# Optimization experiments

Hardware: AMD Instinct MI355X
Metric: run time of the kernel (lower is better)

## Reference

```python
import jax, jax.numpy as jnp
import numpy as np

FEATURE_DIM = 256
NUM_HEADS = 4
HEAD_DIM = FEATURE_DIM // NUM_HEADS  # 64
B, N = 4, 2048


def _conv1x1(x, w, b):
    # x: [B, C_in, N], w: [C_out, C_in], b: [C_out] -> [B, C_out, N]
    return jnp.einsum('oc,bcn->bon', w, x) + b[None, :, None]


def setup_inputs() -> dict:
    key = jax.random.key(0)
    ks = jax.random.split(key, 11)
    std = 0.02
    d = {
        'query': jax.random.normal(ks[0], (B, FEATURE_DIM, N), jnp.float32),
        'key': jax.random.normal(ks[1], (B, FEATURE_DIM, N), jnp.float32),
        'value': jax.random.normal(ks[2], (B, FEATURE_DIM, N), jnp.float32),
        'wq': jax.random.normal(ks[3], (FEATURE_DIM, FEATURE_DIM), jnp.float32) * std,
        'bq': jnp.zeros((FEATURE_DIM,), jnp.float32),
        'wk': jax.random.normal(ks[4], (FEATURE_DIM, FEATURE_DIM), jnp.float32) * std,
        'bk': jnp.zeros((FEATURE_DIM,), jnp.float32),
        'wv': jax.random.normal(ks[5], (FEATURE_DIM, FEATURE_DIM), jnp.float32) * std,
        'bv': jnp.zeros((FEATURE_DIM,), jnp.float32),
        'wm': jax.random.normal(ks[6], (FEATURE_DIM, FEATURE_DIM), jnp.float32) * std,
        'bm': jnp.zeros((FEATURE_DIM,), jnp.float32),
    }
    return d


def reference(query, key, value, wq, bq, wk, bk, wv, bv, wm, bm):
    b = query.shape[0]
    # 1x1 conv projections, then split channels as (head_dim, num_heads) -- head_dim outer,
    # matching torch's .view(b, head_dim, num_heads, -1)
    q = _conv1x1(query, wq, bq).reshape(b, HEAD_DIM, NUM_HEADS, -1)
    k = _conv1x1(key, wk, bk).reshape(b, HEAD_DIM, NUM_HEADS, -1)
    v = _conv1x1(value, wv, bv).reshape(b, HEAD_DIM, NUM_HEADS, -1)
    scores = jnp.einsum('bdhn,bdhm->bhnm', q, k) / jnp.sqrt(jnp.asarray(HEAD_DIM, q.dtype))
    probs = jax.nn.softmax(scores, axis=-1)
    out = jnp.einsum('bhnm,bdhm->bdhn', probs, v)
    out = out.reshape(b, HEAD_DIM * NUM_HEADS, -1)
    return _conv1x1(out, wm, bm)
```

## Files before the change

### kernel.cpp

```cpp
#include <hip/hip_runtime.h>
#include <math.h>

#define B_ 4
#define C_ 256
#define N_ 2048
#define H_ 4
#define D_ 64

typedef __attribute__((ext_vector_type(8))) short bf16x8;
typedef __attribute__((ext_vector_type(4))) float f32x4;

#define QSCALE 0.18033688011112042f

__device__ __forceinline__ float fexp2(float x) {
#if __has_builtin(__builtin_amdgcn_exp2f)
    return __builtin_amdgcn_exp2f(x);
#else
    float r;
    asm("v_exp_f32 %0, %1\n\ts_nop 1" : "=v"(r) : "v"(x));
    return r;
#endif
}

__device__ __forceinline__ ushort f2bf(float x) {
    uint u = __float_as_uint(x);
    uint r = (u + 0x7fffu + ((u >> 16) & 1u)) >> 16;
    return (ushort)r;
}
__device__ __forceinline__ float bf2f(ushort u) {
    return __uint_as_float((uint)u << 16);
}
__device__ __forceinline__ uint4 pack8(const ushort* v) {
    uint4 r;
    r.x = (uint)v[0] | ((uint)v[1] << 16);
    r.y = (uint)v[2] | ((uint)v[3] << 16);
    r.z = (uint)v[4] | ((uint)v[5] << 16);
    r.w = (uint)v[6] | ((uint)v[7] << 16);
    return r;
}
__device__ __forceinline__ void glds16(const void* g, void* l) {
    __builtin_amdgcn_global_load_lds(
        (const __attribute__((address_space(1))) unsigned int*)g,
        (__attribute__((address_space(3))) unsigned int*)l, 16, 0, 0);
}

__global__ __launch_bounds__(256) void pack_w(const float* __restrict__ w0,
                                              const float* __restrict__ w1,
                                              const float* __restrict__ w2,
                                              const float* __restrict__ w3,
                                              ushort* __restrict__ Whimg,
                                              ushort* __restrict__ Wlimg) {
    const int ws = blockIdx.x;
    const int ks = blockIdx.y;
    const float* W = ws == 0 ? w0 : ws == 1 ? w1 : ws == 2 ? w2 : w3;
    ushort* Hh = Whimg + ws * 65536;
    ushort* Hl = Wlimg + ws * 65536;
    const int o  = threadIdx.x;
    const int of = o >> 4;
    const int li = o & 15;

    float v[32];
#pragma unroll
    for (int q = 0; q < 8; ++q)
        *(float4*)&v[q * 4] = *(const float4*)&W[o * 256 + ks * 32 + q * 4];

#pragma unroll
    for (int g = 0; g < 4; ++g) {
        ushort hi[8], lo[8];
#pragma unroll
        for (int e = 0; e < 8; ++e) {
            const float x = v[g * 8 + e];
            hi[e] = f2bf(x);
            lo[e] = f2bf(x - bf2f(hi[e]));
        }
        const size_t dst = ((size_t)(ks * 16 + of) * 64 + (g * 16 + li)) * 8;
        *(uint4*)(Hh + dst) = pack8(hi);
        if (ws == 3) *(uint4*)(Hl + dst) = pack8(lo);
    }
}

__global__ __launch_bounds__(256) void proj_fused(const float* __restrict__ Xq,
                                                  const float* __restrict__ Xk,
                                                  const float* __restrict__ Xv,
                                                  const ushort* __restrict__ Whimg,
                                                  const float* __restrict__ bq,
                                                  const float* __restrict__ bk,
                                                  const float* __restrict__ bv,
                                                  ushort* __restrict__ Qb,
                                                  ushort* __restrict__ Kimg,
                                                  ushort* __restrict__ Vimg) {
    __shared__ float  Xf[2][2048];
    __shared__ ushort Xb[2][2048];
    __shared__ ushort Ls[32][264];

    const int z   = blockIdx.z;
    const int sel = z >> 2, b = z & 3;
    const int nt  = blockIdx.x;
    const int n0  = nt * 32;
    const int tid  = threadIdx.x;
    const int wv   = tid >> 6;
    const int lane = tid & 63;
    const int li   = lane & 15;
    const int g    = lane >> 4;
    const int l7   = li & 7;

    const float* X = (sel == 0 ? Xq : sel == 1 ? Xk : Xv) + (size_t)b * C_ * N_;
    const ushort* Wh  = Whimg + sel * 65536;
    const float* bias = sel == 0 ? bq : sel == 1 ? bk : bv;

    const int st_row = wv * 16 + (lane >> 3);
    const int st_col = (lane & 7) * 4;

    const int cv_n  = tid & 31;
    const int cv_g  = tid >> 5;
    const int cv_c0 = cv_g * 8;
    const int cv_sl = (cv_g ^ (cv_n & 7)) * 8;

#define PSTAGE(buf, s_)                                                          \
    do {                                                                         \
        const float* p_ = X + (size_t)((s_) * 64 + st_row) * N_ + n0 + st_col;   \
        glds16(p_,          &Xf[buf][wv * 512]);                                 \
        glds16(p_ + 8 * N_, &Xf[buf][wv * 512 + 256]);                           \
    } while (0)

#define PCONV(dst, src)                                                          \
    do {                                                                         \
        ushort t_[8];                                                            \
        _Pragma("unroll")                                                        \
        for (int e = 0; e < 8; ++e)                                              \
            t_[e] = f2bf(Xf[src][(cv_c0 + e) * 32 + cv_n]);                      \
        *(uint4*)&Xb[dst][cv_n * 64 + cv_sl] = pack8(t_);                        \
    } while (0)

    PSTAGE(0, 0);
    __syncthreads();
    PSTAGE(1, 1);
    PCONV(0, 0);
    __syncthreads();

    const f32x4 zv = {0.f, 0.f, 0.f, 0.f};
    f32x4 acc[4][2] = {{zv, zv}, {zv, zv}, {zv, zv}, {zv, zv}};

    for (int st = 0; st < 4; ++st) {
        if (st + 2 < 4) PSTAGE(st & 1, st + 2);
        if (st + 1 < 4) PCONV((st + 1) & 1, (st + 1) & 1);

        bf16x8 xb[2][2];
#pragma unroll
        for (int nf = 0; nf < 2; ++nf)
#pragma unroll
            for (int ksub = 0; ksub < 2; ++ksub)
                xb[nf][ksub] = *(const bf16x8*)
                    &Xb[st & 1][(16 * nf + li) * 64 + 8 * (((ksub << 2) + g) ^ l7)];

        __builtin_amdgcn_s_setprio(1);
#pragma unroll
        for (int ksub = 0; ksub < 2; ++ksub) {
            const size_t ab = ((size_t)((2 * st + ksub) * 16 + wv * 4) * 64 + lane) * 8;
#pragma unroll
            for (int ot = 0; ot < 4; ++ot) {
                const bf16x8 ah = *(const bf16x8*)(Wh + ab + (size_t)ot * 512);
#pragma unroll
                for (int nf = 0; nf < 2; ++nf)
                    acc[ot][nf] = __builtin_amdgcn_mfma_f32_16x16x32_bf16(
                        ah, xb[nf][ksub], acc[ot][nf], 0, 0, 0);
            }
        }
        __builtin_amdgcn_s_setprio(0);
        __syncthreads();
    }

    const float scale = (sel == 0) ? QSCALE : 1.0f;
#pragma unroll
    for (int ot = 0; ot < 4; ++ot)
#pragma unroll
        for (int nf = 0; nf < 2; ++nf)
#pragma unroll
            for (int r = 0; r < 4; ++r) {
                const int o = wv * 64 + ot * 16 + g * 4 + r;
                Ls[nf * 16 + li][o] = f2bf((acc[ot][nf][r] + bias[o]) * scale);
            }
    __syncthreads();

    const int h  = tid >> 6;
    const int bh = b * 4 + h;
    if (sel == 0) {
#pragma unroll
        for (int r_ = 0; r_ < 4; ++r_) {
            const int gi = (tid & 63) + 64 * r_;
            const int n_l = gi >> 3, dr = gi & 7;
            ushort u[8];
#pragma unroll
            for (int e = 0; e < 8; ++e) u[e] = Ls[n_l][(dr * 8 + e) * 4 + h];
            *(uint4*)(Qb + (((size_t)bh * N_) + n0 + n_l) * 64 + dr * 8) = pack8(u);
        }
    } else if (sel == 1) {
#pragma unroll
        for (int r_ = 0; r_ < 4; ++r_) {
            const int gi = (tid & 63) + 64 * r_;
            const int n_l = gi >> 3, dr = gi & 7;
            ushort u[8];
#pragma unroll
            for (int e = 0; e < 8; ++e) u[e] = Ls[n_l][(dr * 8 + e) * 4 + h];
            const int jg    = n0 + n_l;
            const int j     = jg & 63;
            const int ktile = jg >> 6;
            *(uint4*)(Kimg + (((size_t)bh * 32 + ktile) << 12) + j * 64 +
                      ((dr * 8) ^ ((j & 7) << 3))) = pack8(u);
        }
    } else {
#pragma unroll
        for (int r_ = 0; r_ < 4; ++r_) {
            const int gi = (tid & 63) + 64 * r_;
            const int d = gi >> 2, jr = gi & 3;
            ushort u[8];
#pragma unroll
            for (int e = 0; e < 8; ++e) u[e] = Ls[jr * 8 + e][d * 4 + h];
            const int jbase = (nt & 1) * 32 + jr * 8;
            const int ktile = nt >> 1;
            *(uint4*)(Vimg + (((size_t)bh * 32 + ktile) << 12) + d * 64 +
                      (jbase ^ ((d & 7) << 3))) = pack8(u);
        }
    }
#undef PSTAGE
#undef PCONV
}

__global__ __launch_bounds__(256) void attn_v8(const ushort* __restrict__ Qb,
                                               const ushort* __restrict__ Kimg,
                                               const ushort* __restrict__ Vimg,
                                               float* __restrict__ Opart,
                                               float* __restrict__ lpart) {
    __shared__ ushort SMEM[24576];

    const int bid = blockIdx.x;
    const int L   = (bid & 7) * 64 + (bid >> 3);
    const int qt  = L & 15;
    const int ps  = L >> 4;
    const int bh  = ps >> 1;
    const int s   = ps & 1;

    const int tid  = threadIdx.x;
    const int wv   = tid >> 6;
    const int lane = tid & 63;
    const int li   = lane & 15;
    const int g    = lane >> 4;
    const int l7   = li & 7;
    const int i0w  = qt * 128 + wv * 32;

    bf16x8 qf[2][2];
#pragma unroll
    for (int qg = 0; qg < 2; ++qg)
#pragma unroll
        for (int ks = 0; ks < 2; ++ks)
            qf[qg][ks] = *(const bf16x8*)(Qb + ((size_t)bh * N_ + i0w + qg * 16 + li) * 64 +
                                          ks * 32 + g * 8);

    const ushort* Kg = Kimg + ((size_t)bh << 17);
    const ushort* Vg = Vimg + ((size_t)bh << 17);
    ushort* Pw = SMEM + 16384 + wv * 2048;

    const f32x4 z = {0.f, 0.f, 0.f, 0.f};
    f32x4 accO[4][2] = {{z, z}, {z, z}, {z, z}, {z, z}};
    f32x4 accL[2] = {z, z};
    const bf16x8 ones = {16256, 16256, 16256, 16256, 16256, 16256, 16256, 16256};

    const int kt0 = s * 16, kt1 = kt0 + 16;

#define STAGE(buf, kt_)                                                          \
    do {                                                                         \
        const ushort* ksrc = Kg + ((size_t)(kt_) << 12) + wv * 1024 + lane * 8;  \
        const ushort* vsrc = Vg + ((size_t)(kt_) << 12) + wv * 1024 + lane * 8;  \
        glds16(ksrc,       SMEM + (buf) * 4096 + wv * 1024);                     \
        glds16(ksrc + 512, SMEM + (buf) * 4096 + wv * 1024 + 512);               \
        glds16(vsrc,       SMEM + 8192 + (buf) * 4096 + wv * 1024);              \
        glds16(vsrc + 512, SMEM + 8192 + (buf) * 4096 + wv * 1024 + 512);        \
    } while (0)

    STAGE(0, kt0);

    int cur = 0;
    for (int kt = kt0; kt < kt1; ++kt) {
        if (kt + 1 < kt1) {
            STAGE(cur ^ 1, kt + 1);
            asm volatile("s_waitcnt vmcnt(4)" ::: "memory");
        } else {
            asm volatile("s_waitcnt vmcnt(0)" ::: "memory");
        }
        __builtin_amdgcn_s_barrier();

        const ushort* Kc = SMEM + cur * 4096;
        const ushort* Vc = SMEM + 8192 + cur * 4096;

        f32x4 sc[4][2];
        __builtin_amdgcn_s_setprio(1);
#pragma unroll
        for (int jt = 0; jt < 4; ++jt) {
            const ushort* row = Kc + (16 * jt + li) * 64;
            const bf16x8 kf0 = *(const bf16x8*)(row + 8 * (g ^ l7));
            const bf16x8 kf1 = *(const bf16x8*)(row + 8 * ((4 + g) ^ l7));
#pragma unroll
            for (int qg = 0; qg < 2; ++qg) {
                f32x4 a = z;
                a = __builtin_amdgcn_mfma_f32_16x16x32_bf16(kf0, qf[qg][0], a, 0, 0, 0);
                a = __builtin_amdgcn_mfma_f32_16x16x32_bf16(kf1, qf[qg][1], a, 0, 0, 0);
                sc[jt][qg] = a;
            }
        }
        __builtin_amdgcn_s_setprio(0);

#pragma unroll
        for (int qg = 0; qg < 2; ++qg) {
            const uint rowb = (uint)((qg * 16 + li) * 128);
#pragma unroll
            for (int jt = 0; jt < 4; ++jt) {
                const float p0 = fexp2(sc[jt][qg][0]);
                const float p1 = fexp2(sc[jt][qg][1]);
                const float p2 = fexp2(sc[jt][qg][2]);
                const float p3 = fexp2(sc[jt][qg][3]);
                const uint a01 = (__float_as_uint(p1) & 0xffff0000u) | (__float_as_uint(p0) >> 16);
                const uint a23 = (__float_as_uint(p3) & 0xffff0000u) | (__float_as_uint(p2) >> 16);
                const uint byteoff = rowb + (((uint)(jt * 32 + g * 8)) ^ ((uint)l7 << 4));
                *(uint2*)((char*)Pw + byteoff) = make_uint2(a01, a23);
            }
        }

        bf16x8 pf[2][2];
#pragma unroll
        for (int qg = 0; qg < 2; ++qg)
#pragma unroll
            for (int ks = 0; ks < 2; ++ks)
                pf[qg][ks] = *(const bf16x8*)((char*)Pw + (qg * 16 + li) * 128 +
                                              16 * ((4 * ks + g) ^ l7));

        __builtin_amdgcn_s_setprio(1);
#pragma unroll
        for (int qg = 0; qg < 2; ++qg) {
            accL[qg] = __builtin_amdgcn_mfma_f32_16x16x32_bf16(ones, pf[qg][0], accL[qg], 0, 0, 0);
            accL[qg] = __builtin_amdgcn_mfma_f32_16x16x32_bf16(ones, pf[qg][1], accL[qg], 0, 0, 0);
        }

#pragma unroll
        for (int dt = 0; dt < 4; ++dt) {
            const ushort* row = Vc + (16 * dt + li) * 64;
            const bf16x8 vf0 = *(const bf16x8*)(row + 8 * (g ^ l7));
            const bf16x8 vf1 = *(const bf16x8*)(row + 8 * ((4 + g) ^ l7));
#pragma unroll
            for (int qg = 0; qg < 2; ++qg) {
                f32x4 a = accO[dt][qg];
                a = __builtin_amdgcn_mfma_f32_16x16x32_bf16(vf0, pf[qg][0], a, 0, 0, 0);
                a = __builtin_amdgcn_mfma_f32_16x16x32_bf16(vf1, pf[qg][1], a, 0, 0, 0);
                accO[dt][qg] = a;
            }
        }
        __builtin_amdgcn_s_setprio(0);

        __builtin_amdgcn_s_barrier();
        cur ^= 1;
    }
#undef STAGE

    const int sbase = (s * 16 + bh) * 128 + qt * 8 + wv * 2;
#pragma unroll
    for (int qg = 0; qg < 2; ++qg) {
        const int slot = sbase + qg;
        float* Op = Opart + (size_t)slot * 1024;
#pragma unroll
        for (int dt = 0; dt < 4; ++dt)
            *(f32x4*)&Op[li * 64 + dt * 16 + g * 4] = accO[dt][qg];
        if (g == 0) lpart[slot * 16 + li] = accL[qg][0];
    }
}

__global__ __launch_bounds__(256) void conv_out(const float* __restrict__ Opart,
                                                const float* __restrict__ lpart,
                                                const ushort* __restrict__ Whimg,
                                                const ushort* __restrict__ Wlimg,
                                                const float* __restrict__ bm,
                                                float* __restrict__ out) {
    __shared__ ushort Bh[512 * 8];
    __shared__ ushort Bl[512 * 8];
    __shared__ float Linv[4][16];

    const int bx  = blockIdx.x;
    const int b   = blockIdx.y;
    const int n0  = bx * 16;
    const int qt  = bx >> 2;
    const int wq  = bx & 3;
    const int tid = threadIdx.x;

    if (tid < 64) {
        const int h = tid >> 4, q = tid & 15;
        const int sl0 = (((0 * 16 + b * 4 + h) * 32 + qt) * 4 + wq);
        const int sl1 = (((1 * 16 + b * 4 + h) * 32 + qt) * 4 + wq);
        Linv[h][q] = 1.0f / (lpart[sl0 * 16 + q] + lpart[sl1 * 16 + q]);
    }
    __syncthreads();

#pragma unroll
    for (int it = 0; it < 4; ++it) {
        const int id = tid + 256 * it;
        const int h  = id >> 8;
        const int q  = (id >> 4) & 15;
        const int d4 = id & 15;
        const size_t sl0 = (size_t)(((0 * 16 + b * 4 + h) * 32 + qt) * 4 + wq);
        const size_t sl1 = (size_t)(((1 * 16 + b * 4 + h) * 32 + qt) * 4 + wq);
        const f32x4 v0 = *(const f32x4*)&Opart[sl0 * 1024 + q * 64 + d4 * 4];
        const f32x4 v1 = *(const f32x4*)&Opart[sl1 * 1024 + q * 64 + d4 * 4];
        const float li_ = Linv[h][q];
#pragma unroll
        for (int e = 0; e < 4; ++e) {
            const int d = d4 * 4 + e;
            const float vv = (v0[e] + v1[e]) * li_;
            const ushort hi = f2bf(vv);
            const ushort lo = f2bf(vv - bf2f(hi));
            const int cg = d >> 1;
            const int eb = (d & 1) * 4 + h;
            const int Gp = (q * 32 + cg) ^ (q & 7);
            Bh[Gp * 8 + eb] = hi;
            Bl[Gp * 8 + eb] = lo;
        }
    }
    __syncthreads();

    const int wv = tid >> 6, lane = tid & 63, li = lane & 15, g = lane >> 4;
    const ushort* Wh = Whimg + 3 * 65536;
    const ushort* Wl = Wlimg + 3 * 65536;
    const f32x4 zv = {0.f, 0.f, 0.f, 0.f};
    f32x4 acc[4] = {zv, zv, zv, zv};

    for (int ks = 0; ks < 8; ++ks) {
        const int Gp = (li * 32 + ks * 4 + g) ^ (li & 7);
        const bf16x8 bh_ = *(const bf16x8*)(Bh + Gp * 8);
        const bf16x8 bl_ = *(const bf16x8*)(Bl + Gp * 8);
        const size_t abase = ((size_t)(ks * 16 + wv * 4) * 64 + lane) * 8;
#pragma unroll
        for (int ot = 0; ot < 4; ++ot) {
            const bf16x8 ah = *(const bf16x8*)(Wh + abase + (size_t)ot * 512);
            const bf16x8 al = *(const bf16x8*)(Wl + abase + (size_t)ot * 512);
            f32x4 a = acc[ot];
            a = __builtin_amdgcn_mfma_f32_16x16x32_bf16(ah, bl_, a, 0, 0, 0);
            a = __builtin_amdgcn_mfma_f32_16x16x32_bf16(al, bh_, a, 0, 0, 0);
            a = __builtin_amdgcn_mfma_f32_16x16x32_bf16(ah, bh_, a, 0, 0, 0);
            acc[ot] = a;
        }
    }

#pragma unroll
    for (int ot = 0; ot < 4; ++ot)
#pragma unroll
        for (int r = 0; r < 4; ++r) {
            const int o = wv * 64 + ot * 16 + g * 4 + r;
            out[((size_t)(b * 256 + o)) * N_ + n0 + li] = acc[ot][r] + bm[o];
        }
}

extern "C" void kernel_launch(void* const* d_in, const int* in_sizes, int n_in,
                              void* d_out, int out_size, void* d_ws, size_t ws_size,
                              hipStream_t stream) {
    const float* query = (const float*)d_in[0];
    const float* key   = (const float*)d_in[1];
    const float* value = (const float*)d_in[2];
    const float* wq = (const float*)d_in[3];
    const float* bq = (const float*)d_in[4];
    const float* wk = (const float*)d_in[5];
    const float* bk = (const float*)d_in[6];
    const float* wv = (const float*)d_in[7];
    const float* bv = (const float*)d_in[8];
    const float* wm = (const float*)d_in[9];
    const float* bm = (const float*)d_in[10];

    float* out = (float*)d_out;
    char*  ws  = (char*)d_ws;

    const size_t TEN = (size_t)B_ * C_ * N_;

    float*  Opart = (float*)ws;
    float*  lpart = (float*)(ws + (size_t)4096 * 1024 * 4);
    ushort* Qb    = (ushort*)(ws + (size_t)4096 * 1024 * 4 + 262144);
    ushort* Kimg  = Qb + TEN;
    ushort* Vimg  = Kimg + TEN;
    ushort* Whimg = Vimg + TEN;
    ushort* Wlimg = Whimg + 4 * 65536;

    pack_w<<<dim3(4, 8), dim3(256), 0, stream>>>(wq, wk, wv, wm, Whimg, Wlimg);
    proj_fused<<<dim3(64, 1, 12), dim3(256), 0, stream>>>(query, key, value,
                                                          Whimg, bq, bk, bv,
                                                          Qb, Kimg, Vimg);
    attn_v8<<<dim3(512), dim3(256), 0, stream>>>(Qb, Kimg, Vimg, Opart, lpart);
    conv_out<<<dim3(128, 4), dim3(256), 0, stream>>>(Opart, lpart, Whimg, Wlimg, bm, out);
}
```

Baseline: 62.02 us.

## Compute softmax row sums on VALU and retile output conv for weight reuse

The attention kernel drops the two MFMA ops per query group that multiplied P by a ones vector to get row sums. Instead it accumulates the fp32 exponentials in registers and reduces them across lane groups with shuffles at the end, which removes matrix-core work from the inner loop but adds VALU adds. The output conv now uses 32-column tiles and splits output channels across a grid z dimension, so each weight fragment load feeds two MFMA column tiles. Row sums now come from unrounded fp32 values rather than bf16-rounded P, which changes numerics slightly.

```diff
diff --git a/kernel.cpp b/kernel.cpp
--- a/kernel.cpp
+++ b/kernel.cpp
@@ -226,7 +226,7 @@
 #undef PCONV
 }
 
-__global__ __launch_bounds__(256) void attn_v8(const ushort* __restrict__ Qb,
+__global__ __launch_bounds__(256) void attn_v9(const ushort* __restrict__ Qb,
                                                const ushort* __restrict__ Kimg,
                                                const ushort* __restrict__ Vimg,
                                                float* __restrict__ Opart,
@@ -262,8 +262,7 @@
 
     const f32x4 z = {0.f, 0.f, 0.f, 0.f};
     f32x4 accO[4][2] = {{z, z}, {z, z}, {z, z}, {z, z}};
-    f32x4 accL[2] = {z, z};
-    const bf16x8 ones = {16256, 16256, 16256, 16256, 16256, 16256, 16256, 16256};
+    float lsum[2] = {0.f, 0.f};
 
     const int kt0 = s * 16, kt1 = kt0 + 16;
 
@@ -318,6 +317,7 @@
                 const float p1 = fexp2(sc[jt][qg][1]);
                 const float p2 = fexp2(sc[jt][qg][2]);
                 const float p3 = fexp2(sc[jt][qg][3]);
+                lsum[qg] += (p0 + p1) + (p2 + p3);
                 const uint a01 = (__float_as_uint(p1) & 0xffff0000u) | (__float_as_uint(p0) >> 16);
                 const uint a23 = (__float_as_uint(p3) & 0xffff0000u) | (__float_as_uint(p2) >> 16);
                 const uint byteoff = rowb + (((uint)(jt * 32 + g * 8)) ^ ((uint)l7 << 4));
@@ -334,12 +334,6 @@
                                               16 * ((4 * ks + g) ^ l7));
 
         __builtin_amdgcn_s_setprio(1);
-#pragma unroll
-        for (int qg = 0; qg < 2; ++qg) {
-            accL[qg] = __builtin_amdgcn_mfma_f32_16x16x32_bf16(ones, pf[qg][0], accL[qg], 0, 0, 0);
-            accL[qg] = __builtin_amdgcn_mfma_f32_16x16x32_bf16(ones, pf[qg][1], accL[qg], 0, 0, 0);
-        }
-
 #pragma unroll
         for (int dt = 0; dt < 4; ++dt) {
             const ushort* row = Vc + (16 * dt + li) * 64;
@@ -368,7 +362,10 @@
 #pragma unroll
         for (int dt = 0; dt < 4; ++dt)
             *(f32x4*)&Op[li * 64 + dt * 16 + g * 4] = accO[dt][qg];
-        if (g == 0) lpart[slot * 16 + li] = accL[qg][0];
+        float l0 = lsum[qg];
+        l0 += __shfl_xor(l0, 16);
+        l0 += __shfl_xor(l0, 32);
+        if (g == 0) lpart[slot * 16 + li] = l0;
     }
 }
 
@@ -378,40 +375,46 @@
                                                 const ushort* __restrict__ Wlimg,
                                                 const float* __restrict__ bm,
                                                 float* __restrict__ out) {
-    __shared__ ushort Bh[512 * 8];
-    __shared__ ushort Bl[512 * 8];
-    __shared__ float Linv[4][16];
+    __shared__ ushort Bh[1024 * 8];
+    __shared__ ushort Bl[1024 * 8];
+    __shared__ float Linv[4][32];
 
     const int bx  = blockIdx.x;
     const int b   = blockIdx.y;
-    const int n0  = bx * 16;
-    const int qt  = bx >> 2;
-    const int wq  = bx & 3;
+    const int oh  = blockIdx.z;
+    const int n0  = bx * 32;
     const int tid = threadIdx.x;
 
-    if (tid < 64) {
-        const int h = tid >> 4, q = tid & 15;
-        const int sl0 = (((0 * 16 + b * 4 + h) * 32 + qt) * 4 + wq);
-        const int sl1 = (((1 * 16 + b * 4 + h) * 32 + qt) * 4 + wq);
-        Linv[h][q] = 1.0f / (lpart[sl0 * 16 + q] + lpart[sl1 * 16 + q]);
+    if (tid < 128) {
+        const int h = tid >> 5, q = tid & 31;
+        const int gq  = (n0 + q) >> 4;
+        const int qi  = q & 15;
+        const int sl0 = (0 * 16 + b * 4 + h) * 128 + gq;
+        const int sl1 = (1 * 16 + b * 4 + h) * 128 + gq;
+        Linv[h][q] = 1.0f / (lpart[sl0 * 16 + qi] + lpart[sl1 * 16 + qi]);
     }
     __syncthreads();
 
 #pragma unroll
     for (int it = 0; it < 4; ++it) {
         const int id = tid + 256 * it;
-        const int h  = id >> 8;
-        const int q  = (id >> 4) & 15;
-        const int d4 = id & 15;
-        const size_t sl0 = (size_t)(((0 * 16 + b * 4 + h) * 32 + qt) * 4 + wq);
-        const size_t sl1 = (size_t)(((1 * 16 + b * 4 + h) * 32 + qt) * 4 + wq);
-        const f32x4 v0 = *(const f32x4*)&Opart[sl0 * 1024 + q * 64 + d4 * 4];
-        const f32x4 v1 = *(const f32x4*)&Opart[sl1 * 1024 + q * 64 + d4 * 4];
+        const int q  = (id & 7) | (((id >> 6) & 3) << 3);
+        const int h  = (id >> 3) & 3;
+        const int d0 = (((id >> 5) & 1) | (((id >> 8) & 3) << 1)) * 8;
+        const int gq = (n0 + q) >> 4;
+        const int qi = (n0 + q) & 15;
+        const size_t sl0 = (size_t)((0 * 16 + b * 4 + h) * 128 + gq);
+        const size_t sl1 = (size_t)((1 * 16 + b * 4 + h) * 128 + gq);
+        const f32x4 v0a = *(const f32x4*)&Opart[sl0 * 1024 + qi * 64 + d0];
+        const f32x4 v0b = *(const f32x4*)&Opart[sl0 * 1024 + qi * 64 + d0 + 4];
+        const f32x4 v1a = *(const f32x4*)&Opart[sl1 * 1024 + qi * 64 + d0];
+        const f32x4 v1b = *(const f32x4*)&Opart[sl1 * 1024 + qi * 64 + d0 + 4];
         const float li_ = Linv[h][q];
 #pragma unroll
-        for (int e = 0; e < 4; ++e) {
-            const int d = d4 * 4 + e;
-            const float vv = (v0[e] + v1[e]) * li_;
+        for (int e = 0; e < 8; ++e) {
+            const int d = d0 + e;
+            const float vv = ((e < 4 ? v0a[e & 3] : v0b[e & 3]) +
+                              (e < 4 ? v1a[e & 3] : v1b[e & 3])) * li_;
             const ushort hi = f2bf(vv);
             const ushort lo = f2bf(vv - bf2f(hi));
             const int cg = d >> 1;
@@ -427,32 +430,43 @@
     const ushort* Wh = Whimg + 3 * 65536;
     const ushort* Wl = Wlimg + 3 * 65536;
     const f32x4 zv = {0.f, 0.f, 0.f, 0.f};
-    f32x4 acc[4] = {zv, zv, zv, zv};
+    f32x4 acc[2][2] = {{zv, zv}, {zv, zv}};
 
     for (int ks = 0; ks < 8; ++ks) {
-        const int Gp = (li * 32 + ks * 4 + g) ^ (li & 7);
-        const bf16x8 bh_ = *(const bf16x8*)(Bh + Gp * 8);
-        const bf16x8 bl_ = *(const bf16x8*)(Bl + Gp * 8);
-        const size_t abase = ((size_t)(ks * 16 + wv * 4) * 64 + lane) * 8;
-#pragma unroll
-        for (int ot = 0; ot < 4; ++ot) {
-            const bf16x8 ah = *(const bf16x8*)(Wh + abase + (size_t)ot * 512);
-            const bf16x8 al = *(const bf16x8*)(Wl + abase + (size_t)ot * 512);
-            f32x4 a = acc[ot];
-            a = __builtin_amdgcn_mfma_f32_16x16x32_bf16(ah, bl_, a, 0, 0, 0);
-            a = __builtin_amdgcn_mfma_f32_16x16x32_bf16(al, bh_, a, 0, 0, 0);
-            a = __builtin_amdgcn_mfma_f32_16x16x32_bf16(ah, bh_, a, 0, 0, 0);
-            acc[ot] = a;
-        }
-    }
-
-#pragma unroll
-    for (int ot = 0; ot < 4; ++ot)
-#pragma unroll
-        for (int r = 0; r < 4; ++r) {
-            const int o = wv * 64 + ot * 16 + g * 4 + r;
-            out[((size_t)(b * 256 + o)) * N_ + n0 + li] = acc[ot][r] + bm[o];
-        }
+        bf16x8 bhf[2], blf[2];
+#pragma unroll
+        for (int nf = 0; nf < 2; ++nf) {
+            const int Gp = (((16 * nf + li) * 32) + ks * 4 + g) ^ (li & 7);
+            bhf[nf] = *(const bf16x8*)(Bh + Gp * 8);
+            blf[nf] = *(const bf16x8*)(Bl + Gp * 8);
+        }
+#pragma unroll
+        for (int ot = 0; ot < 2; ++ot) {
+            const int of = oh * 8 + wv * 2 + ot;
+            const size_t abase = ((size_t)(ks * 16 + of) * 64 + lane) * 8;
+            const bf16x8 ah = *(const bf16x8*)(Wh + abase);
+            const bf16x8 al = *(const bf16x8*)(Wl + abase);
+#pragma unroll
+            for (int nf = 0; nf < 2; ++nf) {
+                f32x4 a = acc[ot][nf];
+                a = __builtin_amdgcn_mfma_f32_16x16x32_bf16(ah, blf[nf], a, 0, 0, 0);
+                a = __builtin_amdgcn_mfma_f32_16x16x32_bf16(al, bhf[nf], a, 0, 0, 0);
+                a = __builtin_amdgcn_mfma_f32_16x16x32_bf16(ah, bhf[nf], a, 0, 0, 0);
+                acc[ot][nf] = a;
+            }
+        }
+    }
+
+#pragma unroll
+    for (int ot = 0; ot < 2; ++ot)
+#pragma unroll
+        for (int nf = 0; nf < 2; ++nf)
+#pragma unroll
+            for (int r = 0; r < 4; ++r) {
+                const int o = oh * 128 + wv * 32 + ot * 16 + g * 4 + r;
+                out[((size_t)(b * 256 + o)) * N_ + n0 + nf * 16 + li] =
+                    acc[ot][nf][r] + bm[o];
+            }
 }
 
 extern "C" void kernel_launch(void* const* d_in, const int* in_sizes, int n_in,
@@ -487,6 +501,6 @@
     proj_fused<<<dim3(64, 1, 12), dim3(256), 0, stream>>>(query, key, value,
                                                           Whimg, bq, bk, bv,
                                                           Qb, Kimg, Vimg);
-    attn_v8<<<dim3(512), dim3(256), 0, stream>>>(Qb, Kimg, Vimg, Opart, lpart);
-    conv_out<<<dim3(128, 4), dim3(256), 0, stream>>>(Opart, lpart, Whimg, Wlimg, bm, out);
-}
+    attn_v9<<<dim3(512), dim3(256), 0, stream>>>(Qb, Kimg, Vimg, Opart, lpart);
+    conv_out<<<dim3(64, 4, 2), dim3(256), 0, stream>>>(Opart, lpart, Whimg, Wlimg, bm, out);
+}
```

Result: slower. 64.83 us (+4.5%).
